# Optimization experiments

Hardware: AMD Instinct MI355X
Metric: run time of the kernel (lower is better)

The kernel has to match this reference:

```python
import jax, jax.numpy as jnp
import numpy as np

H = 16          # num_heads
DH = 128        # head_dim
TILE = 128      # tile_size
TOPK = 8        # top_k_tiles
NEG = -1e10


def _rotate_half(x):
    half = x.shape[-1] // 2
    return jnp.concatenate([-x[..., half:], x[..., :half]], axis=-1)


def setup_inputs() -> dict:
    key = jax.random.key(0)
    B, S, D = 2, 2048, H * DH
    ks = jax.random.split(key, 5)
    x = jax.random.normal(ks[0], (B, S, D), dtype=jnp.float32)
    scale = 0.02
    wq = jax.random.normal(ks[1], (D, H * DH), dtype=jnp.float32) * scale
    wk = jax.random.normal(ks[2], (D, H * DH), dtype=jnp.float32) * scale
    wv = jax.random.normal(ks[3], (D, H * DH), dtype=jnp.float32) * scale
    wo = jax.random.normal(ks[4], (H * DH, D), dtype=jnp.float32) * scale
    # RoPE tables: freqs_cis.real / .imag, shape [S, head_dim//2]
    inv_freq = 1.0 / (10000.0 ** (np.arange(0, DH, 2, dtype=np.float32) / DH))
    angles = np.arange(S, dtype=np.float32)[:, None] * inv_freq[None, :]
    cos = jnp.asarray(np.cos(angles), dtype=jnp.float32)
    sin = jnp.asarray(np.sin(angles), dtype=jnp.float32)
    return {"x": x, "wq": wq, "wk": wk, "wv": wv, "wo": wo, "cos": cos, "sin": sin}


def reference(x, wq, wk, wv, wo, cos, sin):
    B, S, D = x.shape
    # QKV projections -> [B, H, S, Dh]
    q = (x @ wq).reshape(B, S, H, DH).transpose(0, 2, 1, 3)
    k = (x @ wk).reshape(B, S, H, DH).transpose(0, 2, 1, 3)
    v = (x @ wv).reshape(B, S, H, DH).transpose(0, 2, 1, 3)
    # RoPE (half-split / rotate_half form), in fp32 as in source
    cf = jnp.concatenate([cos, cos], axis=-1)[None, None].astype(jnp.float32)  # [1,1,S,Dh]
    sf = jnp.concatenate([sin, sin], axis=-1)[None, None].astype(jnp.float32)
    q = q.astype(jnp.float32)
    k = k.astype(jnp.float32)
    q = q * cf + _rotate_half(q) * sf
    k = k * cf + _rotate_half(k) * sf
    # Full causal logits [B,H,S,S] (short-seq branch: seq_len <= 8192)
    scale = 1.0 / jnp.sqrt(jnp.float32(DH))
    logits = jnp.einsum('bhqd,bhkd->bhqk', q, k) * scale
    causal = jnp.tril(jnp.ones((S, S), dtype=bool))
    logits = jnp.where(causal[None, None], logits, NEG)
    # Tile scoring: softmax over representative rows, tile max-pool, top-k tiles
    num_tiles = S // TILE
    rep_pos = jnp.arange(TILE - 1, S, TILE)           # last query of each tile
    rep_w = jax.nn.softmax(logits[:, :, rep_pos, :], axis=-1)  # [B,H,nt,S]
    tile_scores = jnp.max(rep_w.reshape(B, H, num_tiles, num_tiles, TILE), axis=-1)
    _, group_tile_indices = jax.lax.top_k(tile_scores, min(TOPK, num_tiles))  # [B,H,nt,topk]
    # Full causal attention (explicit path, same math as dot_product_attention is_causal)
    weights = jax.nn.softmax(logits, axis=-1)
    out = jnp.einsum('bhqk,bhkd->bhqd', weights, v)
    out = out.transpose(0, 2, 1, 3).reshape(B, S, H * DH)
    out = out @ wo
    return out, group_tile_indices
```

## Files before the change

kernel.cpp:

```cpp
#include <hip/hip_runtime.h>
#include <cstdint>
#include <cstddef>


#define S_LEN 2048
#define NH 16
#define DHD 128
#define DMODEL 2048
#define MROWS 4096
#define SCALE 0.08838834764831845f
#define SCALE_L2E (0.08838834764831845f * 1.4426950408889634f)
#define NEG10 -1e10f

typedef short short8 __attribute__((ext_vector_type(8)));
typedef __bf16 bf16x8 __attribute__((ext_vector_type(8)));
typedef float f32x4 __attribute__((ext_vector_type(4)));

#define MFMA16(a, b, c) __builtin_amdgcn_mfma_f32_16x16x32_bf16((a), (b), (c), 0, 0, 0)

__device__ __forceinline__ void gl16(const void* g, void* s) {
  __builtin_amdgcn_global_load_lds(
      (const __attribute__((address_space(1))) void*)g,
      (__attribute__((address_space(3))) void*)s, 16, 0, 0);
}

__device__ __forceinline__ unsigned short f2bf(float f) {
  unsigned u = __float_as_uint(f);
  return (unsigned short)((u + 0x7fffu + ((u >> 16) & 1u)) >> 16);
}
__device__ __forceinline__ float bf2f(unsigned short h) {
  return __uint_as_float(((unsigned)h) << 16);
}

__global__ __launch_bounds__(256) void k_split_x(const float* __restrict__ x,
                                                 unsigned short* __restrict__ xh,
                                                 unsigned short* __restrict__ xl, int n4) {
  int i = blockIdx.x * blockDim.x + threadIdx.x;
  for (; i < n4; i += gridDim.x * blockDim.x) {
    float4 v = ((const float4*)x)[i];
    float f[4] = {v.x, v.y, v.z, v.w};
    unsigned short hh[4], ll[4];
#pragma unroll
    for (int j = 0; j < 4; j++) {
      hh[j] = f2bf(f[j]);
      ll[j] = f2bf(f[j] - bf2f(hh[j]));
    }
    ((ushort4*)xh)[i] = make_ushort4(hh[0], hh[1], hh[2], hh[3]);
    ((ushort4*)xl)[i] = make_ushort4(ll[0], ll[1], ll[2], ll[3]);
  }
}

template <int LO>
__global__ __launch_bounds__(256) void k_transw(const float* __restrict__ w,
                                                unsigned short* __restrict__ th,
                                                unsigned short* __restrict__ tl) {
  int n = blockIdx.x * 256 + threadIdx.x;
  int r0 = blockIdx.y * 32;
  float vals[32];
#pragma unroll
  for (int j = 0; j < 32; j++) vals[j] = w[(size_t)(r0 + j) * DMODEL + n];
  unsigned short hs[32];
#pragma unroll
  for (int j = 0; j < 32; j++) hs[j] = f2bf(vals[j]);
  unsigned short* dsth = th + (size_t)n * DMODEL + r0;
#pragma unroll
  for (int c = 0; c < 4; c++) {
    short8 v;
#pragma unroll
    for (int j = 0; j < 8; j++) v[j] = (short)hs[c * 8 + j];
    *(short8*)(dsth + c * 8) = v;
  }
  if (LO) {
    unsigned short ls[32];
#pragma unroll
    for (int j = 0; j < 32; j++) ls[j] = f2bf(vals[j] - bf2f(hs[j]));
    unsigned short* dstl = tl + (size_t)n * DMODEL + r0;
#pragma unroll
    for (int c = 0; c < 4; c++) {
      short8 v;
#pragma unroll
      for (int j = 0; j < 8; j++) v[j] = (short)ls[c * 8 + j];
      *(short8*)(dstl + c * 8) = v;
    }
  }
}

template <int SPLIT, int EPI>
__global__ __launch_bounds__(256) void k_gemm(const unsigned short* __restrict__ A,
                                              const unsigned short* __restrict__ Al,
                                              const unsigned short* __restrict__ Bt,
                                              const unsigned short* __restrict__ Btl,
                                              void* __restrict__ outp) {
  constexpr int NSM = (SPLIT ? 4 : 2) * 4096;
  __shared__ unsigned short sm[NSM];
  unsigned short* sAh = sm;
  unsigned short* sAl = SPLIT ? (sm + 4096) : nullptr;
  unsigned short* sBh = sm + (SPLIT ? 8192 : 4096);
  unsigned short* sBl = SPLIT ? (sm + 12288) : nullptr;

  const int tid = threadIdx.x;
  const int l = tid & 63, w = tid >> 6;
  const int lr = l & 15, lk = l >> 4;
  const int rowBase = blockIdx.y * 128;
  const int colBase = blockIdx.x * 128;
  const int wr = (w >> 1) * 64, wc = (w & 1) * 64;

  f32x4 zero = {0.f, 0.f, 0.f, 0.f};
  f32x4 acc[4][4];
#pragma unroll
  for (int mi = 0; mi < 4; mi++)
#pragma unroll
    for (int ni = 0; ni < 4; ni++) acc[mi][ni] = zero;

  for (int kt = 0; kt < 64; ++kt) {
#pragma unroll
    for (int p = 0; p < 2; ++p) {
      int c = w * 128 + p * 64 + l;
      int row = c >> 2, sl = c & 3;
      int kbl = sl ^ ((row >> 1) & 3);
      size_t srca = (size_t)(rowBase + row) * DMODEL + kt * 32 + kbl * 8;
      gl16(A + srca, (char*)sAh + c * 16);
      if (SPLIT) gl16(Al + srca, (char*)sAl + c * 16);
      size_t srcb = (size_t)(colBase + row) * DMODEL + kt * 32 + kbl * 8;
      gl16(Bt + srcb, (char*)sBh + c * 16);
      if (SPLIT) gl16(Btl + srcb, (char*)sBl + c * 16);
    }
    __syncthreads();

    bf16x8 ah[4], alo[4], bh[4], blo[4];
#pragma unroll
    for (int mi = 0; mi < 4; mi++) {
      int row = wr + mi * 16 + lr;
      int off = row * 32 + ((lk ^ ((row >> 1) & 3)) * 8);
      ah[mi] = *(const bf16x8*)(sAh + off);
      if (SPLIT) alo[mi] = *(const bf16x8*)(sAl + off);
    }
#pragma unroll
    for (int ni = 0; ni < 4; ni++) {
      int row = wc + ni * 16 + lr;
      int off = row * 32 + ((lk ^ ((row >> 1) & 3)) * 8);
      bh[ni] = *(const bf16x8*)(sBh + off);
      if (SPLIT) blo[ni] = *(const bf16x8*)(sBl + off);
    }
#pragma unroll
    for (int mi = 0; mi < 4; mi++)
#pragma unroll
      for (int ni = 0; ni < 4; ni++) {
        acc[mi][ni] = MFMA16(ah[mi], bh[ni], acc[mi][ni]);
        if (SPLIT) {
          acc[mi][ni] = MFMA16(alo[mi], bh[ni], acc[mi][ni]);
          acc[mi][ni] = MFMA16(ah[mi], blo[ni], acc[mi][ni]);
        }
      }
    __syncthreads();
  }

#pragma unroll
  for (int mi = 0; mi < 4; mi++)
#pragma unroll
    for (int ni = 0; ni < 4; ni++)
#pragma unroll
      for (int r = 0; r < 4; r++) {
        int row = rowBase + wr + mi * 16 + lk * 4 + r;
        int col = colBase + wc + ni * 16 + lr;
        float v = acc[mi][ni][r];
        if (EPI == 2) {
          ((float*)outp)[(size_t)row * DMODEL + col] = v;
        } else {
          size_t idx = (((size_t)(row >> 11) * NH + (col >> 7)) * S_LEN + (row & 2047)) * DHD +
                       (col & 127);
          if (EPI == 1)
            ((float*)outp)[idx] = v;
          else
            ((unsigned short*)outp)[idx] = f2bf(v);
        }
      }
}

__global__ __launch_bounds__(256) void k_rope_q(unsigned short* __restrict__ q,
                                                const float* __restrict__ cosT,
                                                const float* __restrict__ sinT) {
  int t = blockIdx.x * blockDim.x + threadIdx.x;
  int row = t >> 4;
  int i4 = (t & 15) * 4;
  int s = row & 2047;
  unsigned short* p0 = q + (size_t)row * DHD + i4;
  unsigned short* p1 = p0 + 64;
  ushort4 a = *(ushort4*)p0, b = *(ushort4*)p1;
  float4 c = *(const float4*)(cosT + (size_t)s * 64 + i4);
  float4 sn = *(const float4*)(sinT + (size_t)s * 64 + i4);
  float av[4] = {bf2f(a.x), bf2f(a.y), bf2f(a.z), bf2f(a.w)};
  float bv[4] = {bf2f(b.x), bf2f(b.y), bf2f(b.z), bf2f(b.w)};
  float cv[4] = {c.x, c.y, c.z, c.w}, sv[4] = {sn.x, sn.y, sn.z, sn.w};
  unsigned short na[4], nb[4];
#pragma unroll
  for (int j = 0; j < 4; j++) {
    na[j] = f2bf(av[j] * cv[j] - bv[j] * sv[j]);
    nb[j] = f2bf(bv[j] * cv[j] + av[j] * sv[j]);
  }
  *(ushort4*)p0 = make_ushort4(na[0], na[1], na[2], na[3]);
  *(ushort4*)p1 = make_ushort4(nb[0], nb[1], nb[2], nb[3]);
}

__global__ __launch_bounds__(256) void k_rope_k(float* __restrict__ kf,
                                                unsigned short* __restrict__ kb,
                                                const float* __restrict__ cosT,
                                                const float* __restrict__ sinT) {
  int t = blockIdx.x * blockDim.x + threadIdx.x;
  int row = t >> 4;
  int i4 = (t & 15) * 4;
  int s = row & 2047;
  float* p0 = kf + (size_t)row * DHD + i4;
  float* p1 = p0 + 64;
  float4 a = *(float4*)p0, b = *(float4*)p1;
  float4 c = *(const float4*)(cosT + (size_t)s * 64 + i4);
  float4 sn = *(const float4*)(sinT + (size_t)s * 64 + i4);
  float av[4] = {a.x, a.y, a.z, a.w}, bv[4] = {b.x, b.y, b.z, b.w};
  float cv[4] = {c.x, c.y, c.z, c.w}, sv[4] = {sn.x, sn.y, sn.z, sn.w};
  float na[4], nb[4];
#pragma unroll
  for (int j = 0; j < 4; j++) {
    na[j] = av[j] * cv[j] - bv[j] * sv[j];
    nb[j] = bv[j] * cv[j] + av[j] * sv[j];
  }
  *(float4*)p0 = make_float4(na[0], na[1], na[2], na[3]);
  *(float4*)p1 = make_float4(nb[0], nb[1], nb[2], nb[3]);
  unsigned short* kb0 = kb + (size_t)row * DHD + i4;
  *(ushort4*)kb0 = make_ushort4(f2bf(na[0]), f2bf(na[1]), f2bf(na[2]), f2bf(na[3]));
  *(ushort4*)(kb0 + 64) = make_ushort4(f2bf(nb[0]), f2bf(nb[1]), f2bf(nb[2]), f2bf(nb[3]));
}

__global__ __launch_bounds__(256) void k_vtrans(const unsigned short* __restrict__ v,
                                                unsigned short* __restrict__ vt) {
  int bh = blockIdx.y;
  int s0 = blockIdx.x * 64 + (threadIdx.x >> 7) * 32;
  int d = threadIdx.x & 127;
  unsigned short tmp[32];
#pragma unroll
  for (int j = 0; j < 32; j++) tmp[j] = v[((size_t)bh * S_LEN + s0 + j) * DHD + d];
  unsigned short* dst = vt + ((size_t)bh * DHD + d) * S_LEN + s0;
#pragma unroll
  for (int c = 0; c < 4; c++) {
    short8 x;
#pragma unroll
    for (int j = 0; j < 8; j++) x[j] = (short)tmp[c * 8 + j];
    *(short8*)(dst + c * 8) = x;
  }
}

__device__ __forceinline__ void attn_qk_sm(const bf16x8 (&qf)[4], f32x4 (&acc)[8],
                                           float (&mrow)[4], float (&lsum)[4],
                                           const unsigned short* sK, __bf16* sP,
                                           int ktbase, bool diag, int q0, int w, int lr,
                                           int lk) {
  f32x4 zero = {0.f, 0.f, 0.f, 0.f};
  f32x4 sf[4];
#pragma unroll
  for (int nk = 0; nk < 4; nk++) {
    f32x4 sacc = zero;
#pragma unroll
    for (int kd = 0; kd < 4; kd++) {
      int row = nk * 16 + lr;
      int off = row * 128 + (((kd * 4 + lk) ^ (row & 7)) * 8);
      bf16x8 kfrag = *(const bf16x8*)(sK + off);
      sacc = MFMA16(qf[kd], kfrag, sacc);
    }
    sf[nk] = sacc;
  }
#pragma unroll
  for (int r = 0; r < 4; r++) {
    int qpos = q0 + w * 16 + lk * 4 + r;
    float lg[4];
    float mx = -3e38f;
#pragma unroll
    for (int nk = 0; nk < 4; nk++) {
      int kpos = ktbase + nk * 16 + lr;
      float vsc = sf[nk][r] * SCALE_L2E;
      if (diag && kpos > qpos) vsc = -3e38f;
      lg[nk] = vsc;
      mx = fmaxf(mx, vsc);
    }
#pragma unroll
    for (int d = 1; d < 16; d <<= 1) mx = fmaxf(mx, __shfl_xor(mx, d));
    if (mx > mrow[r]) {
      float corr = exp2f(mrow[r] - mx);
      mrow[r] = mx;
      lsum[r] *= corr;
#pragma unroll
      for (int ni = 0; ni < 8; ni++) acc[ni][r] *= corr;
    }
    float m = mrow[r];
    float ps = 0.f;
    int prow = w * 16 + lk * 4 + r;
#pragma unroll
    for (int nk = 0; nk < 4; nk++) {
      float pv = exp2f(lg[nk] - m);
      ps += pv;
      sP[prow * 72 + nk * 16 + lr] = (__bf16)pv;
    }
    lsum[r] += ps;
  }
}

__device__ __forceinline__ void attn_pv(f32x4 (&acc)[8], const __bf16* sP,
                                        const unsigned short* sV, int w, int lr, int lk) {
  bf16x8 pa[2];
#pragma unroll
  for (int ks = 0; ks < 2; ks++) {
    int row = w * 16 + lr;
    pa[ks] = *(const bf16x8*)(sP + row * 72 + ks * 32 + lk * 8);
  }
#pragma unroll
  for (int ni = 0; ni < 8; ni++) {
#pragma unroll
    for (int ks = 0; ks < 2; ks++) {
      int row = ni * 16 + lr;
      int off = row * 64 + (((ks * 4 + lk) ^ (row & 7)) * 8);
      bf16x8 vf = *(const bf16x8*)(sV + off);
      acc[ni] = MFMA16(pa[ks], vf, acc[ni]);
    }
  }
}

__global__ __launch_bounds__(256, 2) void k_attn(const unsigned short* __restrict__ q,
                                                 const unsigned short* __restrict__ k,
                                                 const unsigned short* __restrict__ vt,
                                                 unsigned short* __restrict__ o) {
  __shared__ unsigned short sK[64 * 128];
  __shared__ unsigned short sV[128 * 64];
  __shared__ __bf16 sPA[64 * 72];
  __shared__ __bf16 sPB[64 * 72];

  const int bid = blockIdx.x;
  const int workid = (bid & 7) * 64 + (bid >> 3);
  const int bh = workid >> 4, p = workid & 15;
  const int qtA = p, qtB = 31 - p;
  const int b = bh >> 4, h = bh & 15;
  const int tid = threadIdx.x, l = tid & 63, w = tid >> 6;
  const int lr = l & 15, lk = l >> 4;
  const int q0A = qtA * 64, q0B = qtB * 64;
  const size_t kvbase = (size_t)bh * S_LEN * DHD;

  bf16x8 qfA[4], qfB[4];
#pragma unroll
  for (int kd = 0; kd < 4; kd++) {
    qfA[kd] = *(const bf16x8*)(q + kvbase + (size_t)(q0A + w * 16 + lr) * DHD + kd * 32 + lk * 8);
    qfB[kd] = *(const bf16x8*)(q + kvbase + (size_t)(q0B + w * 16 + lr) * DHD + kd * 32 + lk * 8);
  }

  f32x4 zero = {0.f, 0.f, 0.f, 0.f};
  f32x4 accA[8], accB[8];
  float mrowA[4], lsumA[4], mrowB[4], lsumB[4];
#pragma unroll
  for (int ni = 0; ni < 8; ni++) { accA[ni] = zero; accB[ni] = zero; }
#pragma unroll
  for (int r = 0; r < 4; r++) {
    mrowA[r] = -3e38f; lsumA[r] = 0.f;
    mrowB[r] = -3e38f; lsumB[r] = 0.f;
  }

  for (int kt = 0; kt <= qtB; ++kt) {
#pragma unroll
    for (int pp = 0; pp < 4; ++pp) {
      int c = pp * 256 + tid;
      int kp = c >> 4, sl = c & 15;
      int sls = sl ^ (kp & 7);
      gl16(k + kvbase + (size_t)(kt * 64 + kp) * DHD + sls * 8, (char*)sK + c * 16);
    }
#pragma unroll
    for (int pp = 0; pp < 4; ++pp) {
      int c = pp * 256 + tid;
      int dh = c >> 3, sl = c & 7;
      int sls = sl ^ (dh & 7);
      gl16(vt + ((size_t)bh * DHD + dh) * S_LEN + kt * 64 + sls * 8, (char*)sV + c * 16);
    }
    __syncthreads();

    const bool doA = (kt <= qtA);
    attn_qk_sm(qfB, accB, mrowB, lsumB, sK, sPB, kt * 64, kt == qtB, q0B, w, lr, lk);
    if (doA)
      attn_qk_sm(qfA, accA, mrowA, lsumA, sK, sPA, kt * 64, kt == qtA, q0A, w, lr, lk);
    __syncthreads();

    attn_pv(accB, sPB, sV, w, lr, lk);
    if (doA) attn_pv(accA, sPA, sV, w, lr, lk);
    __syncthreads();
  }

#pragma unroll
  for (int r = 0; r < 4; r++) {
#pragma unroll
    for (int d = 1; d < 16; d <<= 1) {
      lsumA[r] += __shfl_xor(lsumA[r], d);
      lsumB[r] += __shfl_xor(lsumB[r], d);
    }
  }
#pragma unroll
  for (int r = 0; r < 4; r++) {
    float invA = 1.0f / lsumA[r], invB = 1.0f / lsumB[r];
    int srowA = q0A + w * 16 + lk * 4 + r;
    int srowB = q0B + w * 16 + lk * 4 + r;
    size_t baseA = ((size_t)b * S_LEN + srowA) * DMODEL + h * DHD;
    size_t baseB = ((size_t)b * S_LEN + srowB) * DMODEL + h * DHD;
#pragma unroll
    for (int ni = 0; ni < 8; ni++) {
      o[baseA + ni * 16 + lr] = f2bf(accA[ni][r] * invA);
      o[baseB + ni * 16 + lr] = f2bf(accB[ni][r] * invB);
    }
  }
}

__global__ __launch_bounds__(256) void k_score(const float* __restrict__ x,
                                               const float* __restrict__ wq,
                                               const float* __restrict__ cosT,
                                               const float* __restrict__ sinT,
                                               const float* __restrict__ kf,
                                               float* __restrict__ idxout) {
  const int t = blockIdx.x, bh = blockIdx.y;
  const int b = bh >> 4, h = bh & 15;
  const int srep = t * 128 + 127;
  const int tid = threadIdx.x;
  __shared__ float qr[128];
  __shared__ float part[256];
  __shared__ unsigned keys[16];

  {
    const int dh = tid & 127, half = tid >> 7;
    const float* xrow = x + ((size_t)b * S_LEN + srep) * DMODEL;
    const float* wcol = wq + (size_t)h * DHD + dh;
    float s0 = 0.f, s1 = 0.f, s2 = 0.f, s3 = 0.f;
    const int dbase = half * 1024;
    for (int d = 0; d < 1024; d += 4) {
      int dd = dbase + d;
      s0 = fmaf(xrow[dd], wcol[(size_t)dd * DMODEL], s0);
      s1 = fmaf(xrow[dd + 1], wcol[(size_t)(dd + 1) * DMODEL], s1);
      s2 = fmaf(xrow[dd + 2], wcol[(size_t)(dd + 2) * DMODEL], s2);
      s3 = fmaf(xrow[dd + 3], wcol[(size_t)(dd + 3) * DMODEL], s3);
    }
    part[tid] = (s0 + s1) + (s2 + s3);
  }
  if (tid < 16) keys[tid] = ~__float_as_uint(NEG10);
  __syncthreads();
  if (tid < 64) {
    int i = tid;
    float q0v = part[i] + part[i + 128];
    float q1v = part[i + 64] + part[i + 192];
    float c = cosT[(size_t)srep * 64 + i], sn = sinT[(size_t)srep * 64 + i];
    qr[i] = q0v * c - q1v * sn;
    qr[i + 64] = q1v * c + q0v * sn;
  }
  __syncthreads();

  for (int j = tid; j <= srep; j += 256) {
    const float4* krow = (const float4*)(kf + ((size_t)bh * S_LEN + j) * DHD);
    float a0 = 0.f, a1 = 0.f, a2 = 0.f, a3 = 0.f;
#pragma unroll 8
    for (int d4 = 0; d4 < 32; d4++) {
      float4 kv = krow[d4];
      const float* qq = qr + d4 * 4;
      a0 = fmaf(kv.x, qq[0], a0);
      a1 = fmaf(kv.y, qq[1], a1);
      a2 = fmaf(kv.z, qq[2], a2);
      a3 = fmaf(kv.w, qq[3], a3);
    }
    float lg = ((a0 + a1) + (a2 + a3)) * SCALE;
    unsigned u = __float_as_uint(lg);
    unsigned key = (u & 0x80000000u) ? ~u : (u | 0x80000000u);
    atomicMax(&keys[j >> 7], key);
  }
  __syncthreads();

  if (tid == 0) {
    unsigned used = 0;
    float* dst = idxout + ((size_t)bh * 16 + t) * 8;
    for (int r = 0; r < 8; ++r) {
      int best = -1;
      unsigned bk = 0;
#pragma unroll
      for (int tl = 0; tl < 16; ++tl) {
        if (used & (1u << tl)) continue;
        unsigned kv = keys[tl];
        if (best < 0 || kv > bk) {
          bk = kv;
          best = tl;
        }
      }
      used |= (1u << best);
      dst[r] = (float)best;
    }
  }
}

extern "C" void kernel_launch(void* const* d_in, const int* in_sizes, int n_in,
                              void* d_out, int out_size, void* d_ws, size_t ws_size,
                              hipStream_t stream) {
  (void)in_sizes; (void)n_in; (void)out_size; (void)ws_size;
  const float* x = (const float*)d_in[0];
  const float* wq = (const float*)d_in[1];
  const float* wk = (const float*)d_in[2];
  const float* wv = (const float*)d_in[3];
  const float* wo = (const float*)d_in[4];
  const float* cosT = (const float*)d_in[5];
  const float* sinT = (const float*)d_in[6];
  float* out0 = (float*)d_out;
  float* out1 = out0 + (size_t)MROWS * DMODEL;
  float* kf32 = out0;

  char* ws = (char*)d_ws;
  size_t off = 0;
  auto alloc = [&](size_t bytes) {
    void* p = ws + off;
    off += (bytes + 255) & ~(size_t)255;
    return p;
  };
  unsigned short* xh = (unsigned short*)alloc(16777216);
  unsigned short* xl = (unsigned short*)alloc(16777216);
  unsigned short* wqT = (unsigned short*)alloc(8388608);
  unsigned short* wkT = (unsigned short*)alloc(8388608);
  unsigned short* wkTl = (unsigned short*)alloc(8388608);
  unsigned short* wvT = (unsigned short*)alloc(8388608);
  unsigned short* woT = (unsigned short*)alloc(8388608);
  unsigned short* qbf = (unsigned short*)alloc(16777216);
  unsigned short* kbf = (unsigned short*)alloc(16777216);
  unsigned short* vbf = (unsigned short*)alloc(16777216);
  unsigned short* obf = xh;
  unsigned short* vtbf = xl;

  k_split_x<<<2048, 256, 0, stream>>>(x, xh, xl, MROWS * DMODEL / 4);
  dim3 gtw(8, 64);
  k_transw<0><<<gtw, 256, 0, stream>>>(wq, wqT, nullptr);
  k_transw<1><<<gtw, 256, 0, stream>>>(wk, wkT, wkTl);
  k_transw<0><<<gtw, 256, 0, stream>>>(wv, wvT, nullptr);
  k_transw<0><<<gtw, 256, 0, stream>>>(wo, woT, nullptr);

  dim3 gg(16, 32);
  k_gemm<0, 0><<<gg, 256, 0, stream>>>(xh, nullptr, wqT, nullptr, qbf);
  k_gemm<1, 1><<<gg, 256, 0, stream>>>(xh, xl, wkT, wkTl, kf32);
  k_gemm<0, 0><<<gg, 256, 0, stream>>>(xh, nullptr, wvT, nullptr, vbf);

  k_rope_q<<<4096, 256, 0, stream>>>(qbf, cosT, sinT);
  k_rope_k<<<4096, 256, 0, stream>>>(kf32, kbf, cosT, sinT);

  k_vtrans<<<dim3(32, 32), 256, 0, stream>>>(vbf, vtbf);
  k_attn<<<512, 256, 0, stream>>>(qbf, kbf, vtbf, obf);

  k_score<<<dim3(16, 32), 256, 0, stream>>>(x, wq, cosT, sinT, kf32, out1);

  k_gemm<0, 2><<<gg, 256, 0, stream>>>(obf, nullptr, woT, nullptr, out0);
}
```

Measured before the change: 685.1 us.

## Double-buffer K/V tiles in attention and coalesce output stores through LDS

The attention kernel now holds two LDS buffers for K and V. It prefetches the next tile with async global-to-LDS loads while the current tile is computed, waits with partial vmcnt, and drops one barrier per iteration by sharing a single P buffer and running QK then PV per query tile. The epilogue stages normalized outputs in LDS and writes full 16-byte rows to global memory instead of scattered 2-byte stores. LDS use per block grows to roughly 73KB, which could limit occupancy with two blocks per CU.

After: 879.7 us. 28.4% more time.

```diff
diff --git a/kernel.cpp b/kernel.cpp
--- a/kernel.cpp
+++ b/kernel.cpp
@@ -326,10 +326,9 @@
                                                  const unsigned short* __restrict__ k,
                                                  const unsigned short* __restrict__ vt,
                                                  unsigned short* __restrict__ o) {
-  __shared__ unsigned short sK[64 * 128];
-  __shared__ unsigned short sV[128 * 64];
-  __shared__ __bf16 sPA[64 * 72];
-  __shared__ __bf16 sPB[64 * 72];
+  __shared__ unsigned short sK[2][64 * 128];
+  __shared__ unsigned short sV[2][128 * 64];
+  __shared__ __bf16 sP[64 * 72];
 
   const int bid = blockIdx.x;
   const int workid = (bid & 7) * 64 + (bid >> 3);
@@ -359,32 +358,48 @@
     mrowB[r] = -3e38f; lsumB[r] = 0.f;
   }
 
-  for (int kt = 0; kt <= qtB; ++kt) {
+  auto stageV = [&](int kt, int buf) {
+#pragma unroll
+    for (int pp = 0; pp < 4; ++pp) {
+      int c = pp * 256 + tid;
+      int dh = c >> 3, sl = c & 7;
+      int sls = sl ^ (dh & 7);
+      gl16(vt + ((size_t)bh * DHD + dh) * S_LEN + kt * 64 + sls * 8, (char*)sV[buf] + c * 16);
+    }
+  };
+  auto stageK = [&](int kt, int buf) {
 #pragma unroll
     for (int pp = 0; pp < 4; ++pp) {
       int c = pp * 256 + tid;
       int kp = c >> 4, sl = c & 15;
       int sls = sl ^ (kp & 7);
-      gl16(k + kvbase + (size_t)(kt * 64 + kp) * DHD + sls * 8, (char*)sK + c * 16);
-    }
-#pragma unroll
-    for (int pp = 0; pp < 4; ++pp) {
-      int c = pp * 256 + tid;
-      int dh = c >> 3, sl = c & 7;
-      int sls = sl ^ (dh & 7);
-      gl16(vt + ((size_t)bh * DHD + dh) * S_LEN + kt * 64 + sls * 8, (char*)sV + c * 16);
-    }
-    __syncthreads();
+      gl16(k + kvbase + (size_t)(kt * 64 + kp) * DHD + sls * 8, (char*)sK[buf] + c * 16);
+    }
+  };
+
+  stageV(0, 0);
+  stageK(0, 0);
+  int cur = 0;
+
+  for (int kt = 0; kt <= qtB; ++kt) {
+    if (kt < qtB) {
+      stageV(kt + 1, cur ^ 1);
+      stageK(kt + 1, cur ^ 1);
+      asm volatile("s_waitcnt vmcnt(8)" ::: "memory");
+    } else {
+      asm volatile("s_waitcnt vmcnt(0)" ::: "memory");
+    }
+    __builtin_amdgcn_s_barrier();
 
     const bool doA = (kt <= qtA);
-    attn_qk_sm(qfB, accB, mrowB, lsumB, sK, sPB, kt * 64, kt == qtB, q0B, w, lr, lk);
-    if (doA)
-      attn_qk_sm(qfA, accA, mrowA, lsumA, sK, sPA, kt * 64, kt == qtA, q0A, w, lr, lk);
-    __syncthreads();
-
-    attn_pv(accB, sPB, sV, w, lr, lk);
-    if (doA) attn_pv(accA, sPA, sV, w, lr, lk);
-    __syncthreads();
+    attn_qk_sm(qfB, accB, mrowB, lsumB, sK[cur], sP, kt * 64, kt == qtB, q0B, w, lr, lk);
+    attn_pv(accB, sP, sV[cur], w, lr, lk);
+    if (doA) {
+      attn_qk_sm(qfA, accA, mrowA, lsumA, sK[cur], sP, kt * 64, kt == qtA, q0A, w, lr, lk);
+      attn_pv(accA, sP, sV[cur], w, lr, lk);
+    }
+    __builtin_amdgcn_s_barrier();
+    cur ^= 1;
   }
 
 #pragma unroll
@@ -395,17 +410,39 @@
       lsumB[r] += __shfl_xor(lsumB[r], d);
     }
   }
-#pragma unroll
-  for (int r = 0; r < 4; r++) {
-    float invA = 1.0f / lsumA[r], invB = 1.0f / lsumB[r];
-    int srowA = q0A + w * 16 + lk * 4 + r;
-    int srowB = q0B + w * 16 + lk * 4 + r;
-    size_t baseA = ((size_t)b * S_LEN + srowA) * DMODEL + h * DHD;
-    size_t baseB = ((size_t)b * S_LEN + srowB) * DMODEL + h * DHD;
-#pragma unroll
-    for (int ni = 0; ni < 8; ni++) {
-      o[baseA + ni * 16 + lr] = f2bf(accA[ni][r] * invA);
-      o[baseB + ni * 16 + lr] = f2bf(accB[ni][r] * invB);
+
+  unsigned short* sO = (unsigned short*)sK;
+  {
+#pragma unroll
+    for (int r = 0; r < 4; r++) {
+      float inv = 1.0f / lsumB[r];
+      int row = w * 16 + lk * 4 + r;
+#pragma unroll
+      for (int ni = 0; ni < 8; ni++) sO[row * 136 + ni * 16 + lr] = f2bf(accB[ni][r] * inv);
+    }
+    __syncthreads();
+#pragma unroll
+    for (int pass = 0; pass < 4; ++pass) {
+      int idx = pass * 256 + tid;
+      int row = idx >> 4, c8 = (idx & 15) * 8;
+      short8 v = *(short8*)(sO + row * 136 + c8);
+      *(short8*)(o + ((size_t)b * S_LEN + q0B + row) * DMODEL + h * DHD + c8) = v;
+    }
+    __syncthreads();
+#pragma unroll
+    for (int r = 0; r < 4; r++) {
+      float inv = 1.0f / lsumA[r];
+      int row = w * 16 + lk * 4 + r;
+#pragma unroll
+      for (int ni = 0; ni < 8; ni++) sO[row * 136 + ni * 16 + lr] = f2bf(accA[ni][r] * inv);
+    }
+    __syncthreads();
+#pragma unroll
+    for (int pass = 0; pass < 4; ++pass) {
+      int idx = pass * 256 + tid;
+      int row = idx >> 4, c8 = (idx & 15) * 8;
+      short8 v = *(short8*)(sO + row * 136 + c8);
+      *(short8*)(o + ((size_t)b * S_LEN + q0A + row) * DMODEL + h * DHD + c8) = v;
     }
   }
 }
```
